# Kernel optimization log

Measured on AMD Instinct MI355X. Metric: run time of the kernel, lower is better.

The kernel has to match this reference:

```python
import jax, jax.numpy as jnp
import numpy as np

EPS = 1e-6
NUM_HEADS = 8
HEAD_DIM = 64


def _elu_plus_one(x):
    # ELU(x) + 1 : positive feature map used for linear attention
    return jax.nn.elu(x) + 1.0


def setup_inputs() -> dict:
    key = jax.random.key(0)
    ks = jax.random.split(key, 10)
    B, S, D = 1, 4096, 512  # batch, seq_len, hidden_size
    P = NUM_HEADS * HEAD_DIM  # proj_dim == hidden_size here
    scale = 0.05  # keep projections numerically tame
    return {
        "hidden_states": jax.random.normal(ks[0], (B, S, D), jnp.float32),
        "Wq": jax.random.normal(ks[1], (D, P), jnp.float32) * scale,
        "bq": jnp.zeros((P,), jnp.float32),
        "Wk": jax.random.normal(ks[2], (D, P), jnp.float32) * scale,
        "bk": jnp.zeros((P,), jnp.float32),
        "Wv": jax.random.normal(ks[3], (D, P), jnp.float32) * scale,
        "bv": jnp.zeros((P,), jnp.float32),
        "Wo": jax.random.normal(ks[4], (P, D), jnp.float32) * scale,
        # persistent per-head tensor-product memory: M [H, Dh, Dh], z [H, Dh]
        "M_mem": jax.random.uniform(ks[5], (NUM_HEADS, HEAD_DIM, HEAD_DIM), jnp.float32),
        "z_mem": jax.random.uniform(ks[6], (NUM_HEADS, HEAD_DIM), jnp.float32),
    }


def reference(hidden_states, Wq, bq, Wk, bk, Wv, bv, Wo, M_mem, z_mem):
    B, S, D = hidden_states.shape
    H, Dh = NUM_HEADS, HEAD_DIM

    def split_heads(t):
        # [B, S, H*Dh] -> [B, H, S, Dh]
        return t.reshape(B, S, H, Dh).transpose(0, 2, 1, 3)

    q = split_heads(hidden_states @ Wq + bq)
    k = split_heads(hidden_states @ Wk + bk)
    v = split_heads(hidden_states @ Wv + bv)

    sq = _elu_plus_one(q)  # sigma(Q)  [B,H,S,Dh]
    sk = _elu_plus_one(k)  # sigma(K)  [B,H,S,Dh]

    # kv[t] = sigma(k_t) (x) v_t ; causal prefix sums, seeded by persistent memory
    kv = sk[..., :, None] * v[..., None, :]            # [B,H,S,Dh,Dh]
    cumsum_kv = jnp.cumsum(kv, axis=2) + M_mem[None, :, None]  # + M per head
    cumsum_k = jnp.cumsum(sk, axis=2) + z_mem[None, :, None]   # + z per head

    numerator = jnp.einsum('bhsd,bhsde->bhse', sq, cumsum_kv)  # [B,H,S,Dh]
    denominator = jnp.einsum('bhsd,bhsd->bhs', sq, cumsum_k)   # [B,H,S]
    out = numerator / (denominator[..., None] + EPS)

    out = out.transpose(0, 2, 1, 3).reshape(B, S, H * Dh)  # merge heads
    return out @ Wo
```

## Files before the change

kernel.cpp:

```cpp
#include <hip/hip_runtime.h>
#include <hip/hip_bf16.h>
#include <math.h>

#define S_LEN 4096
#define D_HID 512
#define P_DIM 512
#define H_NUM 8
#define DH 64
#define NC 64
#define EPS 1e-6f

typedef __attribute__((ext_vector_type(8))) short short8;
typedef __attribute__((ext_vector_type(4))) float f32x4;
typedef __attribute__((ext_vector_type(4))) unsigned short ushort4v;

static __device__ __forceinline__ float b2f(unsigned short u) {
  return __builtin_bit_cast(float, ((unsigned int)u) << 16);
}
static __device__ __forceinline__ unsigned short f2b(float f) {
  unsigned int u = __builtin_bit_cast(unsigned int, f);
  u = (u + 0x7fff + ((u >> 16) & 1)) >> 16;
  return (unsigned short)u;
}
static __device__ __forceinline__ int swz(int row, int d) {
  return d ^ ((row & 7) << 3);
}

#define GLOAD_LDS16(g, l)                                              \
  __builtin_amdgcn_global_load_lds(                                    \
      (const __attribute__((address_space(1))) unsigned int*)(g),      \
      (__attribute__((address_space(3))) unsigned int*)(l), 16, 0, 0)

#define MFMA16(a, b, c) __builtin_amdgcn_mfma_f32_16x16x32_bf16(a, b, c, 0, 0, 0)

#define VMCNT0 asm volatile("s_waitcnt vmcnt(0)" ::: "memory")

__global__ __launch_bounds__(256) void prep_kernel(
    const float* __restrict__ hs, const float* __restrict__ Wq,
    const float* __restrict__ Wk, const float* __restrict__ Wv,
    const float* __restrict__ Wo, unsigned short* __restrict__ hs_bf,
    unsigned short* __restrict__ WT) {
  __shared__ float t[32][33];
  int bid = blockIdx.x, tid = threadIdx.x;
  if (bid < 2048) {
    int idx = bid * 256 + tid;
    float4 v = ((const float4*)hs)[idx];
    ushort4v o = {f2b(v.x), f2b(v.y), f2b(v.z), f2b(v.w)};
    *(ushort4v*)(hs_bf + (size_t)idx * 4) = o;
  } else {
    int b2 = bid - 2048;
    int z = b2 >> 8, r = b2 & 255;
    const float* src = (z == 0) ? Wq : (z == 1) ? Wk : (z == 2) ? Wv : Wo;
    int bx = (r & 15) * 32;
    int by = (r >> 4) * 32;
    int lx = tid & 31, ly = tid >> 5;
#pragma unroll
    for (int i = 0; i < 4; i++)
      t[ly + i * 8][lx] = src[(size_t)(by + ly + i * 8) * 512 + bx + lx];
    __syncthreads();
#pragma unroll
    for (int i = 0; i < 4; i++) {
      int n = bx + ly + i * 8;
      WT[((size_t)z * 512 + n) * 512 + by + lx] = f2b(t[lx][ly + i * 8]);
    }
  }
}

__global__ __launch_bounds__(256) void proj_kernel(
    const unsigned short* __restrict__ hs_bf,
    const unsigned short* __restrict__ WT, const float* __restrict__ bq,
    const float* __restrict__ bk, const float* __restrict__ bv,
    unsigned short* __restrict__ sqz, unsigned short* __restrict__ skz,
    unsigned short* __restrict__ vTz, float* __restrict__ KVt,
    float* __restrict__ ksum) {
  union U {
    struct {
      unsigned short As[2][64 * 32];
      unsigned short Bs[2][192 * 32];
    } st;
    struct {
      unsigned short skT[64 * 64];
      unsigned short vT[64 * 64];
    } cs;
  };
  __shared__ U u;
  int tid = threadIdx.x, w = tid >> 6, lane = tid & 63;
  int c = blockIdx.x, h = blockIdx.y;
  int fr = lane & 15, kg8 = (lane >> 4) * 8, q4 = (lane >> 4) * 4;
  int ldrow = lane >> 2, ldk = (lane & 3) * 8;

  const unsigned short* Ag =
      hs_bf + (size_t)(c * 64 + w * 16 + ldrow) * 512 + ldk;
  const unsigned short* Bg =
      WT + (size_t)(h * 64 + w * 16 + ldrow) * 512 + ldk;

#define PSTAGE(buf, k0)                                              \
  do {                                                               \
    GLOAD_LDS16(Ag + (k0), u.st.As[buf] + w * 512);                  \
    GLOAD_LDS16(Bg + (k0), u.st.Bs[buf] + w * 512);                  \
    GLOAD_LDS16(Bg + 262144 + (k0), u.st.Bs[buf] + 2048 + w * 512);  \
    GLOAD_LDS16(Bg + 524288 + (k0), u.st.Bs[buf] + 4096 + w * 512);  \
  } while (0)

  f32x4 acc[12] = {};
  PSTAGE(0, 0);
  VMCNT0;
  __builtin_amdgcn_s_barrier();
  int cur = 0;
  for (int it = 0; it < 16; it++) {
    if (it < 15) PSTAGE(cur ^ 1, (it + 1) * 32);
    short8 a = *(const short8*)(u.st.As[cur] + (w * 16 + fr) * 32 + kg8);
#pragma unroll
    for (int nt = 0; nt < 12; nt++) {
      short8 b = *(const short8*)(u.st.Bs[cur] + (nt * 16 + fr) * 32 + kg8);
      acc[nt] = MFMA16(a, b, acc[nt]);
    }
    VMCNT0;
    __builtin_amdgcn_s_barrier();
    cur ^= 1;
  }

#pragma unroll
  for (int nt = 0; nt < 12; nt++) {
    int z = nt >> 2, d = (nt & 3) * 16 + fr;
    float bias = (z == 0) ? bq[h * 64 + d]
                          : (z == 1) ? bk[h * 64 + d] : bv[h * 64 + d];
#pragma unroll
    for (int j = 0; j < 4; j++) {
      int t = w * 16 + q4 + j;
      int s = c * 64 + t;
      float val = acc[nt][j] + bias;
      if (z < 2) val = (val > 0.f) ? (val + 1.f) : __expf(val);
      unsigned short bb = f2b(val);
      if (z == 0) {
        sqz[((size_t)h * S_LEN + s) * 64 + swz(s, d)] = bb;
      } else if (z == 1) {
        skz[((size_t)h * S_LEN + s) * 64 + swz(s, d)] = bb;
        u.cs.skT[d * 64 + swz(d, t)] = bb;
      } else {
        u.cs.vT[d * 64 + swz(d, t)] = bb;
      }
    }
  }
  __syncthreads();

#pragma unroll
  for (int i = 0; i < 2; i++) {
    int G = tid + 256 * i;
    int e = G >> 3, gq = G & 7;
    *(short8*)(vTz + ((size_t)(h * 64 + e)) * S_LEN + c * 64 + gq * 8) =
        *(const short8*)(u.cs.vT + e * 64 + gq * 8);
  }

  {
    short8 onesA = {};
    if (fr == 0) {
#pragma unroll
      for (int j = 0; j < 8; j++) onesA[j] = (short)0x3F80;
    }
    f32x4 accC[4] = {}, accKk[4] = {};
#pragma unroll
    for (int k0 = 0; k0 < 64; k0 += 32) {
      int e = w * 16 + fr;
      short8 a2 =
          *(const short8*)(u.cs.vT + e * 64 + ((k0 + kg8) ^ ((e & 7) << 3)));
#pragma unroll
      for (int nt = 0; nt < 4; nt++) {
        int d = nt * 16 + fr;
        short8 b2 = *(const short8*)(u.cs.skT + d * 64 +
                                     ((k0 + kg8) ^ ((d & 7) << 3)));
        accC[nt] = MFMA16(a2, b2, accC[nt]);
        if (w == 0) accKk[nt] = MFMA16(onesA, b2, accKk[nt]);
      }
    }
    size_t base = (size_t)(h * NC + c) * 4096;
    int e0 = w * 16 + q4;
#pragma unroll
    for (int nt = 0; nt < 4; nt++)
#pragma unroll
      for (int j = 0; j < 4; j++)
        KVt[base + (size_t)(e0 + j) * 64 + nt * 16 + fr] = accC[nt][j];
    if (w == 0 && lane < 16) {
#pragma unroll
      for (int nt = 0; nt < 4; nt++)
        ksum[(size_t)(h * NC + c) * 64 + nt * 16 + lane] = accKk[nt][0];
    }
  }
#undef PSTAGE
}

__global__ __launch_bounds__(256) void prefix2_kernel(
    const float* __restrict__ KVt, const float* __restrict__ ksum,
    const float* __restrict__ M_mem, const float* __restrict__ z_mem,
    unsigned short* __restrict__ KVpz, unsigned short* __restrict__ zp_bf) {
  __shared__ float p[64 * 4];
  __shared__ float zz[64 * 4];
  int h = blockIdx.x >> 6, seg = blockIdx.x & 63;
  int tid = threadIdx.x;
  int d = tid & 63, q = tid >> 6;
  size_t ebase = (size_t)h * NC * 4096 + (size_t)seg * 64 + d;
  float part = 0.f;
#pragma unroll 4
  for (int i = 0; i < 16; i++)
    part += KVt[ebase + (size_t)(q * 16 + i) * 4096];
  p[d * 4 + q] = part;
  if (seg == 0) {
    size_t zb = (size_t)h * NC * 64 + d;
    float pz = 0.f;
#pragma unroll 4
    for (int i = 0; i < 16; i++) pz += ksum[zb + (size_t)(q * 16 + i) * 64];
    zz[d * 4 + q] = pz;
  }
  __syncthreads();
  float pref = M_mem[h * 4096 + d * 64 + seg];
  for (int q2 = 0; q2 < q; q2++) pref += p[d * 4 + q2];
  int sw = swz(seg, d);
#pragma unroll 4
  for (int i = 0; i < 16; i++) {
    int cc = q * 16 + i;
    KVpz[(size_t)(h * NC + cc) * 4096 + seg * 64 + sw] = f2b(pref);
    pref += KVt[ebase + (size_t)cc * 4096];
  }
  if (seg == 0) {
    float bz = z_mem[h * 64 + d];
    for (int q2 = 0; q2 < q; q2++) bz += zz[d * 4 + q2];
    size_t zb = (size_t)h * NC * 64 + d;
#pragma unroll 4
    for (int i = 0; i < 16; i++) {
      int cc = q * 16 + i;
      zp_bf[zb + (size_t)cc * 64] = f2b(bz);
      bz += ksum[zb + (size_t)cc * 64];
    }
  }
}

__global__ __launch_bounds__(256) void attn_mfma(
    const unsigned short* __restrict__ sqz, const unsigned short* __restrict__ skz,
    const unsigned short* __restrict__ vTz, const unsigned short* __restrict__ KVpz,
    const unsigned short* __restrict__ zp_bf, unsigned short* __restrict__ attnb) {
  __shared__ unsigned short sq_lds[4096], sk_lds[4096];
  __shared__ unsigned short btv_lds[80 * 64], btm_lds[80 * 64];
  __shared__ unsigned short shi_lds[4096], slo_lds[4096];
  int h = blockIdx.x / NC, c = blockIdx.x % NC;
  int tid = threadIdx.x, w = tid >> 6, lane = tid & 63;

  {
    const unsigned short* sq_g = sqz + ((size_t)h * S_LEN + c * 64) * 64;
    const unsigned short* sk_g = skz + ((size_t)h * S_LEN + c * 64) * 64;
    const unsigned short* km_g = KVpz + (size_t)(h * NC + c) * 4096;
    int lr = lane >> 3, lc = (lane & 7) * 8;
#pragma unroll
    for (int i = 0; i < 2; i++) {
      int seg = w * 2 + i;
      GLOAD_LDS16(sq_g + seg * 512 + lane * 8, sq_lds + seg * 512);
      GLOAD_LDS16(sk_g + seg * 512 + lane * 8, sk_lds + seg * 512);
      GLOAD_LDS16(km_g + seg * 512 + lane * 8, btm_lds + seg * 512);
      GLOAD_LDS16(vTz + ((size_t)h * 64 + seg * 8 + lr) * S_LEN + c * 64 + lc,
                  btv_lds + seg * 512);
    }
  }
  if (tid < 8) {
    short8 one;
#pragma unroll
    for (int j = 0; j < 8; j++) one[j] = (short)0x3F80;
    *(short8*)(btv_lds + 64 * 64 + tid * 8) = one;
    *(short8*)(btm_lds + 64 * 64 + tid * 8) =
        *(const short8*)(zp_bf + (size_t)(h * NC + c) * 64 + tid * 8);
  }
  __syncthreads();

  int fr = lane & 15, kg8 = (lane >> 4) * 8;
  int ta = w * 16 + fr;
  int sw_a = (ta & 7) << 3;

  f32x4 accS[4] = {};
#pragma unroll
  for (int k0 = 0; k0 < 64; k0 += 32) {
    short8 a = *(const short8*)(sq_lds + ta * 64 + ((k0 + kg8) ^ sw_a));
#pragma unroll
    for (int nt = 0; nt < 4; nt++) {
      int tp = nt * 16 + fr;
      short8 b =
          *(const short8*)(sk_lds + tp * 64 + ((k0 + kg8) ^ ((tp & 7) << 3)));
      accS[nt] = MFMA16(a, b, accS[nt]);
    }
  }
  int r0 = (lane >> 4) * 4;
#pragma unroll
  for (int nt = 0; nt < 4; nt++) {
    int tp = nt * 16 + fr;
#pragma unroll
    for (int j = 0; j < 4; j++) {
      int t = w * 16 + r0 + j;
      float s = (tp <= t) ? accS[nt][j] : 0.f;
      unsigned short hi = f2b(s);
      unsigned short lo = f2b(s - b2f(hi));
      shi_lds[t * 64 + swz(t, tp)] = hi;
      slo_lds[t * 64 + swz(t, tp)] = lo;
    }
  }
  f32x4 acc2[5] = {};
#pragma unroll
  for (int ks = 0; ks < 6; ks++) {
    const unsigned short* asrc = (ks < 2) ? shi_lds : (ks < 4) ? slo_lds : sq_lds;
    const unsigned short* bsrc = (ks < 4) ? btv_lds : btm_lds;
    int ak = (ks & 1) * 32 + kg8;
    short8 a = *(const short8*)(asrc + ta * 64 + (ak ^ sw_a));
#pragma unroll
    for (int nt = 0; nt < 5; nt++) {
      int n = nt * 16 + fr;
      short8 b = *(const short8*)(bsrc + n * 64 + (ak ^ ((n & 7) << 3)));
      acc2[nt] = MFMA16(a, b, acc2[nt]);
    }
  }
  float inv[4];
#pragma unroll
  for (int j = 0; j < 4; j++) {
    float dj = __shfl(acc2[4][j], (lane & 48), 64);
    inv[j] = 1.f / (dj + EPS);
  }
  int srow = c * 64 + w * 16 + r0;
#pragma unroll
  for (int nt = 0; nt < 4; nt++) {
    int col = h * 64 + nt * 16 + fr;
#pragma unroll
    for (int j = 0; j < 4; j++)
      attnb[(size_t)(srow + j) * 512 + col] = f2b(acc2[nt][j] * inv[j]);
  }
}

__global__ __launch_bounds__(256) void gemm_out(
    const unsigned short* __restrict__ A, const unsigned short* __restrict__ BT,
    float* __restrict__ outf) {
  __shared__ unsigned short As[2][64 * 32];
  __shared__ unsigned short Bs[2][128 * 32];
  int tid = threadIdx.x, w = tid >> 6, lane = tid & 63;
  int bm = blockIdx.x * 64, bn = blockIdx.y * 128;
  f32x4 acc[2][4] = {};
  int ldrow = lane >> 2, ldk = (lane & 3) * 8;
  int wr = w >> 1, wc = w & 1;
  int fr = lane & 15, kg8 = (lane >> 4) * 8, q4 = (lane >> 4) * 4;
  const unsigned short* Ag = A + (size_t)(bm + w * 16 + ldrow) * 512 + ldk;
  const unsigned short* Bg0 = BT + (size_t)(bn + w * 16 + ldrow) * 512 + ldk;
  const unsigned short* Bg1 =
      BT + (size_t)(bn + (w + 4) * 16 + ldrow) * 512 + ldk;

#define OSTAGE(buf, k0)                              \
  do {                                               \
    GLOAD_LDS16(Ag + (k0), As[buf] + w * 512);       \
    GLOAD_LDS16(Bg0 + (k0), Bs[buf] + w * 512);      \
    GLOAD_LDS16(Bg1 + (k0), Bs[buf] + (w + 4) * 512); \
  } while (0)

  OSTAGE(0, 0);
  VMCNT0;
  __builtin_amdgcn_s_barrier();
  int cur = 0;
  for (int it = 0; it < 16; it++) {
    if (it < 15) OSTAGE(cur ^ 1, (it + 1) * 32);
    short8 a[2], b[4];
#pragma unroll
    for (int m = 0; m < 2; m++)
      a[m] = *(const short8*)(As[cur] + (wr * 32 + m * 16 + fr) * 32 + kg8);
#pragma unroll
    for (int n = 0; n < 4; n++)
      b[n] = *(const short8*)(Bs[cur] + (wc * 64 + n * 16 + fr) * 32 + kg8);
#pragma unroll
    for (int m = 0; m < 2; m++)
#pragma unroll
      for (int n = 0; n < 4; n++) acc[m][n] = MFMA16(a[m], b[n], acc[m][n]);
    VMCNT0;
    __builtin_amdgcn_s_barrier();
    cur ^= 1;
  }
#pragma unroll
  for (int m = 0; m < 2; m++) {
    int sl0 = wr * 32 + m * 16 + q4;
#pragma unroll
    for (int n = 0; n < 4; n++) {
      int col = bn + wc * 64 + n * 16 + fr;
#pragma unroll
      for (int j = 0; j < 4; j++)
        outf[(size_t)(bm + sl0 + j) * 512 + col] = acc[m][n][j];
    }
  }
#undef OSTAGE
}

extern "C" void kernel_launch(void* const* d_in, const int* in_sizes, int n_in,
                              void* d_out, int out_size, void* d_ws,
                              size_t ws_size, hipStream_t stream) {
  const float* hs = (const float*)d_in[0];
  const float* Wq = (const float*)d_in[1];
  const float* bq = (const float*)d_in[2];
  const float* Wk = (const float*)d_in[3];
  const float* bk = (const float*)d_in[4];
  const float* Wv = (const float*)d_in[5];
  const float* bv = (const float*)d_in[6];
  const float* Wo = (const float*)d_in[7];
  const float* M_mem = (const float*)d_in[8];
  const float* z_mem = (const float*)d_in[9];
  float* out = (float*)d_out;

  unsigned short* hs_bf = (unsigned short*)d_ws;
  unsigned short* WT = hs_bf + (size_t)S_LEN * D_HID;
  unsigned short* sqz = WT + (size_t)4 * 512 * 512;
  unsigned short* skz = sqz + (size_t)H_NUM * S_LEN * DH;
  unsigned short* vTz = skz + (size_t)H_NUM * S_LEN * DH;
  unsigned short* attnb = vTz + (size_t)H_NUM * S_LEN * DH;
  unsigned short* KVpz = attnb + (size_t)S_LEN * P_DIM;
  unsigned short* zp_bf = KVpz + (size_t)H_NUM * NC * DH * DH;
  float* KVt = (float*)(zp_bf + (size_t)H_NUM * NC * DH);
  float* ksum = KVt + (size_t)H_NUM * NC * DH * DH;

  prep_kernel<<<3072, 256, 0, stream>>>(hs, Wq, Wk, Wv, Wo, hs_bf, WT);

  proj_kernel<<<dim3(NC, H_NUM), 256, 0, stream>>>(hs_bf, WT, bq, bk, bv, sqz,
                                                   skz, vTz, KVt, ksum);

  prefix2_kernel<<<512, 256, 0, stream>>>(KVt, ksum, M_mem, z_mem, KVpz, zp_bf);

  attn_mfma<<<512, 256, 0, stream>>>(sqz, skz, vTz, KVpz, zp_bf, attnb);

  gemm_out<<<dim3(S_LEN / 64, 512 / 128), 256, 0, stream>>>(
      attnb, WT + (size_t)3 * 512 * 512, out);
}
```

Measured before the change: 121.1 us.

## Fuse projection, prefix, attention and output GEMM into one persistent kernel

Merges the projection, chunk prefix-sum, intra-chunk attention and output GEMM kernels into one 512-block kernel separated by software grid barriers built on atomics. sq/sk/vT tiles stay in LDS between the projection and attention phases, so their global round-trip is removed, and three kernel launch gaps go away. The projection tile is re-split across warps as 2x6 MFMA tiles and the output GEMM uses 64x64 tiles. The grid barrier assumes all 512 blocks are co-resident, which risks deadlock if occupancy does not allow it. The barriers also serialise phases with spin-waiting.

```diff
diff --git a/kernel.cpp b/kernel.cpp
--- a/kernel.cpp
+++ b/kernel.cpp
@@ -9,6 +9,7 @@
 #define DH 64
 #define NC 64
 #define EPS 1e-6f
+#define NBLK 512
 
 typedef __attribute__((ext_vector_type(8))) short short8;
 typedef __attribute__((ext_vector_type(4))) float f32x4;
@@ -35,13 +36,33 @@
 
 #define VMCNT0 asm volatile("s_waitcnt vmcnt(0)" ::: "memory")
 
+static __device__ __forceinline__ void grid_bar(unsigned* sync, int k) {
+  __syncthreads();
+  if (threadIdx.x == 0) {
+    __threadfence();
+    unsigned prev = __hip_atomic_fetch_add(sync + k, 1u, __ATOMIC_ACQ_REL,
+                                           __HIP_MEMORY_SCOPE_AGENT);
+    if (prev == (unsigned)(NBLK - 1)) {
+      __hip_atomic_store(sync + 4 + k, 1u, __ATOMIC_RELEASE,
+                         __HIP_MEMORY_SCOPE_AGENT);
+    } else {
+      while (__hip_atomic_load(sync + 4 + k, __ATOMIC_ACQUIRE,
+                               __HIP_MEMORY_SCOPE_AGENT) == 0u) {
+        __builtin_amdgcn_s_sleep(2);
+      }
+    }
+  }
+  __syncthreads();
+}
+
 __global__ __launch_bounds__(256) void prep_kernel(
     const float* __restrict__ hs, const float* __restrict__ Wq,
     const float* __restrict__ Wk, const float* __restrict__ Wv,
     const float* __restrict__ Wo, unsigned short* __restrict__ hs_bf,
-    unsigned short* __restrict__ WT) {
+    unsigned short* __restrict__ WT, unsigned* __restrict__ sync) {
   __shared__ float t[32][33];
   int bid = blockIdx.x, tid = threadIdx.x;
+  if (bid == 0 && tid < 8) sync[tid] = 0u;
   if (bid < 2048) {
     int idx = bid * 256 + tid;
     float4 v = ((const float4*)hs)[idx];
@@ -66,93 +87,104 @@
   }
 }
 
-__global__ __launch_bounds__(256) void proj_kernel(
+__global__ __launch_bounds__(256) void fused_kernel(
     const unsigned short* __restrict__ hs_bf,
     const unsigned short* __restrict__ WT, const float* __restrict__ bq,
     const float* __restrict__ bk, const float* __restrict__ bv,
-    unsigned short* __restrict__ sqz, unsigned short* __restrict__ skz,
-    unsigned short* __restrict__ vTz, float* __restrict__ KVt,
-    float* __restrict__ ksum) {
-  union U {
-    struct {
-      unsigned short As[2][64 * 32];
-      unsigned short Bs[2][192 * 32];
-    } st;
-    struct {
-      unsigned short skT[64 * 64];
-      unsigned short vT[64 * 64];
-    } cs;
-  };
-  __shared__ U u;
-  int tid = threadIdx.x, w = tid >> 6, lane = tid & 63;
-  int c = blockIdx.x, h = blockIdx.y;
+    const float* __restrict__ M_mem, const float* __restrict__ z_mem,
+    float* __restrict__ KVt, float* __restrict__ ksum,
+    unsigned short* __restrict__ KVpz, unsigned short* __restrict__ zp_bf,
+    unsigned short* __restrict__ attnb, float* __restrict__ outf,
+    unsigned* __restrict__ sync) {
+  __shared__ unsigned short sqL[64 * 64];
+  __shared__ unsigned short skL[64 * 64];
+  __shared__ unsigned short vTL[80 * 64];
+  __shared__ unsigned short uraw[16384];
+
+  int bid = blockIdx.x, tid = threadIdx.x;
+  int w = tid >> 6, lane = tid & 63;
+  int h = bid & 7, c = bid >> 3;
   int fr = lane & 15, kg8 = (lane >> 4) * 8, q4 = (lane >> 4) * 4;
   int ldrow = lane >> 2, ldk = (lane & 3) * 8;
-
-  const unsigned short* Ag =
-      hs_bf + (size_t)(c * 64 + w * 16 + ldrow) * 512 + ldk;
-  const unsigned short* Bg =
-      WT + (size_t)(h * 64 + w * 16 + ldrow) * 512 + ldk;
-
-#define PSTAGE(buf, k0)                                              \
-  do {                                                               \
-    GLOAD_LDS16(Ag + (k0), u.st.As[buf] + w * 512);                  \
-    GLOAD_LDS16(Bg + (k0), u.st.Bs[buf] + w * 512);                  \
-    GLOAD_LDS16(Bg + 262144 + (k0), u.st.Bs[buf] + 2048 + w * 512);  \
-    GLOAD_LDS16(Bg + 524288 + (k0), u.st.Bs[buf] + 4096 + w * 512);  \
+  int wr = w >> 1, wc = w & 1;
+
+  {
+    const unsigned short* Ag =
+        hs_bf + (size_t)(c * 64 + w * 16 + ldrow) * 512 + ldk;
+    const unsigned short* Bg =
+        WT + (size_t)(h * 64 + w * 16 + ldrow) * 512 + ldk;
+#define PSTAGE(buf, k0)                                                   \
+  do {                                                                    \
+    GLOAD_LDS16(Ag + (k0), uraw + (buf)*2048 + w * 512);                  \
+    GLOAD_LDS16(Bg + (k0), uraw + 4096 + (buf)*6144 + w * 512);           \
+    GLOAD_LDS16(Bg + 262144 + (k0), uraw + 4096 + (buf)*6144 + 2048 + w * 512); \
+    GLOAD_LDS16(Bg + 524288 + (k0), uraw + 4096 + (buf)*6144 + 4096 + w * 512); \
   } while (0)
 
-  f32x4 acc[12] = {};
-  PSTAGE(0, 0);
-  VMCNT0;
-  __builtin_amdgcn_s_barrier();
-  int cur = 0;
-  for (int it = 0; it < 16; it++) {
-    if (it < 15) PSTAGE(cur ^ 1, (it + 1) * 32);
-    short8 a = *(const short8*)(u.st.As[cur] + (w * 16 + fr) * 32 + kg8);
-#pragma unroll
-    for (int nt = 0; nt < 12; nt++) {
-      short8 b = *(const short8*)(u.st.Bs[cur] + (nt * 16 + fr) * 32 + kg8);
-      acc[nt] = MFMA16(a, b, acc[nt]);
-    }
+    f32x4 acc[2][6] = {};
+    PSTAGE(0, 0);
     VMCNT0;
     __builtin_amdgcn_s_barrier();
-    cur ^= 1;
-  }
-
-#pragma unroll
-  for (int nt = 0; nt < 12; nt++) {
-    int z = nt >> 2, d = (nt & 3) * 16 + fr;
-    float bias = (z == 0) ? bq[h * 64 + d]
-                          : (z == 1) ? bk[h * 64 + d] : bv[h * 64 + d];
-#pragma unroll
-    for (int j = 0; j < 4; j++) {
-      int t = w * 16 + q4 + j;
-      int s = c * 64 + t;
-      float val = acc[nt][j] + bias;
-      if (z < 2) val = (val > 0.f) ? (val + 1.f) : __expf(val);
-      unsigned short bb = f2b(val);
-      if (z == 0) {
-        sqz[((size_t)h * S_LEN + s) * 64 + swz(s, d)] = bb;
-      } else if (z == 1) {
-        skz[((size_t)h * S_LEN + s) * 64 + swz(s, d)] = bb;
-        u.cs.skT[d * 64 + swz(d, t)] = bb;
-      } else {
-        u.cs.vT[d * 64 + swz(d, t)] = bb;
-      }
-    }
-  }
-  __syncthreads();
-
-#pragma unroll
-  for (int i = 0; i < 2; i++) {
-    int G = tid + 256 * i;
-    int e = G >> 3, gq = G & 7;
-    *(short8*)(vTz + ((size_t)(h * 64 + e)) * S_LEN + c * 64 + gq * 8) =
-        *(const short8*)(u.cs.vT + e * 64 + gq * 8);
-  }
-
-  {
+    int cur = 0;
+    for (int it = 0; it < 16; it++) {
+      if (it < 15) PSTAGE(cur ^ 1, (it + 1) * 32);
+      short8 a[2], b[6];
+#pragma unroll
+      for (int m = 0; m < 2; m++)
+        a[m] = *(const short8*)(uraw + cur * 2048 +
+                                (wr * 32 + m * 16 + fr) * 32 + kg8);
+#pragma unroll
+      for (int n = 0; n < 6; n++)
+        b[n] = *(const short8*)(uraw + 4096 + cur * 6144 +
+                                (wc * 96 + n * 16 + fr) * 32 + kg8);
+#pragma unroll
+      for (int m = 0; m < 2; m++)
+#pragma unroll
+        for (int n = 0; n < 6; n++) acc[m][n] = MFMA16(a[m], b[n], acc[m][n]);
+      VMCNT0;
+      __builtin_amdgcn_s_barrier();
+      cur ^= 1;
+    }
+#undef PSTAGE
+
+    unsigned short* skT = uraw;
+#pragma unroll
+    for (int n = 0; n < 6; n++) {
+      int cl = wc * 96 + n * 16 + fr;
+      int z = cl >> 6, d = cl & 63;
+      float bias = (z == 0) ? bq[h * 64 + d]
+                            : (z == 1) ? bk[h * 64 + d] : bv[h * 64 + d];
+#pragma unroll
+      for (int m = 0; m < 2; m++) {
+#pragma unroll
+        for (int j = 0; j < 4; j++) {
+          int t = wr * 32 + m * 16 + q4 + j;
+          float val = acc[m][n][j] + bias;
+          if (z < 2) val = (val > 0.f) ? (val + 1.f) : __expf(val);
+          unsigned short bb = f2b(val);
+          if (z == 0) {
+            sqL[t * 64 + swz(t, d)] = bb;
+          } else if (z == 1) {
+            skL[t * 64 + swz(t, d)] = bb;
+            skT[d * 64 + swz(d, t)] = bb;
+          } else {
+            vTL[d * 64 + swz(d, t)] = bb;
+          }
+        }
+      }
+    }
+    if (tid < 8) {
+      short8 one;
+#pragma unroll
+      for (int j = 0; j < 8; j++) one[j] = (short)0x3F80;
+      *(short8*)(vTL + 64 * 64 + tid * 8) = one;
+    }
+    if (tid < 120) {
+      short8 zz = {};
+      *(short8*)(vTL + 65 * 64 + tid * 8) = zz;
+    }
+    __syncthreads();
+
     short8 onesA = {};
     if (fr == 0) {
 #pragma unroll
@@ -163,12 +195,12 @@
     for (int k0 = 0; k0 < 64; k0 += 32) {
       int e = w * 16 + fr;
       short8 a2 =
-          *(const short8*)(u.cs.vT + e * 64 + ((k0 + kg8) ^ ((e & 7) << 3)));
+          *(const short8*)(vTL + e * 64 + ((k0 + kg8) ^ ((e & 7) << 3)));
 #pragma unroll
       for (int nt = 0; nt < 4; nt++) {
         int d = nt * 16 + fr;
-        short8 b2 = *(const short8*)(u.cs.skT + d * 64 +
-                                     ((k0 + kg8) ^ ((d & 7) << 3)));
+        short8 b2 =
+            *(const short8*)(skT + d * 64 + ((k0 + kg8) ^ ((d & 7) << 3)));
         accC[nt] = MFMA16(a2, b2, accC[nt]);
         if (w == 0) accKk[nt] = MFMA16(onesA, b2, accKk[nt]);
       }
@@ -186,205 +218,175 @@
         ksum[(size_t)(h * NC + c) * 64 + nt * 16 + lane] = accKk[nt][0];
     }
   }
-#undef PSTAGE
-}
-
-__global__ __launch_bounds__(256) void prefix2_kernel(
-    const float* __restrict__ KVt, const float* __restrict__ ksum,
-    const float* __restrict__ M_mem, const float* __restrict__ z_mem,
-    unsigned short* __restrict__ KVpz, unsigned short* __restrict__ zp_bf) {
-  __shared__ float p[64 * 4];
-  __shared__ float zz[64 * 4];
-  int h = blockIdx.x >> 6, seg = blockIdx.x & 63;
-  int tid = threadIdx.x;
-  int d = tid & 63, q = tid >> 6;
-  size_t ebase = (size_t)h * NC * 4096 + (size_t)seg * 64 + d;
-  float part = 0.f;
+
+  grid_bar(sync, 0);
+
+  {
+    float* p = (float*)uraw;
+    float* zz = p + 256;
+    int h2 = bid >> 6, seg = bid & 63;
+    int d = tid & 63, q = tid >> 6;
+    size_t ebase = (size_t)h2 * NC * 4096 + (size_t)seg * 64 + d;
+    float part = 0.f;
 #pragma unroll 4
-  for (int i = 0; i < 16; i++)
-    part += KVt[ebase + (size_t)(q * 16 + i) * 4096];
-  p[d * 4 + q] = part;
-  if (seg == 0) {
-    size_t zb = (size_t)h * NC * 64 + d;
-    float pz = 0.f;
+    for (int i = 0; i < 16; i++)
+      part += KVt[ebase + (size_t)(q * 16 + i) * 4096];
+    p[d * 4 + q] = part;
+    if (seg == 0) {
+      size_t zb = (size_t)h2 * NC * 64 + d;
+      float pz = 0.f;
 #pragma unroll 4
-    for (int i = 0; i < 16; i++) pz += ksum[zb + (size_t)(q * 16 + i) * 64];
-    zz[d * 4 + q] = pz;
-  }
-  __syncthreads();
-  float pref = M_mem[h * 4096 + d * 64 + seg];
-  for (int q2 = 0; q2 < q; q2++) pref += p[d * 4 + q2];
-  int sw = swz(seg, d);
-#pragma unroll 4
-  for (int i = 0; i < 16; i++) {
-    int cc = q * 16 + i;
-    KVpz[(size_t)(h * NC + cc) * 4096 + seg * 64 + sw] = f2b(pref);
-    pref += KVt[ebase + (size_t)cc * 4096];
-  }
-  if (seg == 0) {
-    float bz = z_mem[h * 64 + d];
-    for (int q2 = 0; q2 < q; q2++) bz += zz[d * 4 + q2];
-    size_t zb = (size_t)h * NC * 64 + d;
+      for (int i = 0; i < 16; i++) pz += ksum[zb + (size_t)(q * 16 + i) * 64];
+      zz[d * 4 + q] = pz;
+    }
+    __syncthreads();
+    float pref = M_mem[h2 * 4096 + d * 64 + seg];
+    for (int q2 = 0; q2 < q; q2++) pref += p[d * 4 + q2];
+    int sw = swz(seg, d);
 #pragma unroll 4
     for (int i = 0; i < 16; i++) {
       int cc = q * 16 + i;
-      zp_bf[zb + (size_t)cc * 64] = f2b(bz);
-      bz += ksum[zb + (size_t)cc * 64];
-    }
-  }
-}
-
-__global__ __launch_bounds__(256) void attn_mfma(
-    const unsigned short* __restrict__ sqz, const unsigned short* __restrict__ skz,
-    const unsigned short* __restrict__ vTz, const unsigned short* __restrict__ KVpz,
-    const unsigned short* __restrict__ zp_bf, unsigned short* __restrict__ attnb) {
-  __shared__ unsigned short sq_lds[4096], sk_lds[4096];
-  __shared__ unsigned short btv_lds[80 * 64], btm_lds[80 * 64];
-  __shared__ unsigned short shi_lds[4096], slo_lds[4096];
-  int h = blockIdx.x / NC, c = blockIdx.x % NC;
-  int tid = threadIdx.x, w = tid >> 6, lane = tid & 63;
+      KVpz[(size_t)(h2 * NC + cc) * 4096 + seg * 64 + sw] = f2b(pref);
+      pref += KVt[ebase + (size_t)cc * 4096];
+    }
+    if (seg == 0) {
+      float bz = z_mem[h2 * 64 + d];
+      for (int q2 = 0; q2 < q; q2++) bz += zz[d * 4 + q2];
+      size_t zb = (size_t)h2 * NC * 64 + d;
+#pragma unroll 4
+      for (int i = 0; i < 16; i++) {
+        int cc = q * 16 + i;
+        zp_bf[zb + (size_t)cc * 64] = f2b(bz);
+        bz += ksum[zb + (size_t)cc * 64];
+      }
+    }
+  }
+
+  grid_bar(sync, 1);
 
   {
-    const unsigned short* sq_g = sqz + ((size_t)h * S_LEN + c * 64) * 64;
-    const unsigned short* sk_g = skz + ((size_t)h * S_LEN + c * 64) * 64;
+    unsigned short* btm = uraw;
+    unsigned short* shi = uraw + 5120;
+    unsigned short* slo = uraw + 9216;
     const unsigned short* km_g = KVpz + (size_t)(h * NC + c) * 4096;
-    int lr = lane >> 3, lc = (lane & 7) * 8;
 #pragma unroll
     for (int i = 0; i < 2; i++) {
-      int seg = w * 2 + i;
-      GLOAD_LDS16(sq_g + seg * 512 + lane * 8, sq_lds + seg * 512);
-      GLOAD_LDS16(sk_g + seg * 512 + lane * 8, sk_lds + seg * 512);
-      GLOAD_LDS16(km_g + seg * 512 + lane * 8, btm_lds + seg * 512);
-      GLOAD_LDS16(vTz + ((size_t)h * 64 + seg * 8 + lr) * S_LEN + c * 64 + lc,
-                  btv_lds + seg * 512);
-    }
-  }
-  if (tid < 8) {
-    short8 one;
-#pragma unroll
-    for (int j = 0; j < 8; j++) one[j] = (short)0x3F80;
-    *(short8*)(btv_lds + 64 * 64 + tid * 8) = one;
-    *(short8*)(btm_lds + 64 * 64 + tid * 8) =
-        *(const short8*)(zp_bf + (size_t)(h * NC + c) * 64 + tid * 8);
-  }
-  __syncthreads();
-
-  int fr = lane & 15, kg8 = (lane >> 4) * 8;
-  int ta = w * 16 + fr;
-  int sw_a = (ta & 7) << 3;
-
-  f32x4 accS[4] = {};
-#pragma unroll
-  for (int k0 = 0; k0 < 64; k0 += 32) {
-    short8 a = *(const short8*)(sq_lds + ta * 64 + ((k0 + kg8) ^ sw_a));
+      int seg2 = w * 2 + i;
+      GLOAD_LDS16(km_g + seg2 * 512 + lane * 8, btm + seg2 * 512);
+    }
+    if (tid < 8)
+      *(short8*)(btm + 64 * 64 + tid * 8) =
+          *(const short8*)(zp_bf + (size_t)(h * NC + c) * 64 + tid * 8);
+
+    int ta = w * 16 + fr, sw_a = (ta & 7) << 3;
+    f32x4 accS[4] = {};
+#pragma unroll
+    for (int k0 = 0; k0 < 64; k0 += 32) {
+      short8 a = *(const short8*)(sqL + ta * 64 + ((k0 + kg8) ^ sw_a));
+#pragma unroll
+      for (int nt = 0; nt < 4; nt++) {
+        int tp = nt * 16 + fr;
+        short8 b =
+            *(const short8*)(skL + tp * 64 + ((k0 + kg8) ^ ((tp & 7) << 3)));
+        accS[nt] = MFMA16(a, b, accS[nt]);
+      }
+    }
 #pragma unroll
     for (int nt = 0; nt < 4; nt++) {
       int tp = nt * 16 + fr;
-      short8 b =
-          *(const short8*)(sk_lds + tp * 64 + ((k0 + kg8) ^ ((tp & 7) << 3)));
-      accS[nt] = MFMA16(a, b, accS[nt]);
-    }
-  }
-  int r0 = (lane >> 4) * 4;
-#pragma unroll
-  for (int nt = 0; nt < 4; nt++) {
-    int tp = nt * 16 + fr;
+#pragma unroll
+      for (int j = 0; j < 4; j++) {
+        int t = w * 16 + q4 + j;
+        float s = (tp <= t) ? accS[nt][j] : 0.f;
+        unsigned short hi = f2b(s);
+        unsigned short lo = f2b(s - b2f(hi));
+        shi[t * 64 + swz(t, tp)] = hi;
+        slo[t * 64 + swz(t, tp)] = lo;
+      }
+    }
+    __syncthreads();
+    f32x4 acc2[5] = {};
+#pragma unroll
+    for (int ks = 0; ks < 6; ks++) {
+      const unsigned short* asrc = (ks < 2) ? shi : (ks < 4) ? slo : sqL;
+      const unsigned short* bsrc = (ks < 4) ? vTL : btm;
+      int ak = (ks & 1) * 32 + kg8;
+      short8 a = *(const short8*)(asrc + ta * 64 + (ak ^ sw_a));
+#pragma unroll
+      for (int nt = 0; nt < 5; nt++) {
+        int n = nt * 16 + fr;
+        short8 b = *(const short8*)(bsrc + n * 64 + (ak ^ ((n & 7) << 3)));
+        acc2[nt] = MFMA16(a, b, acc2[nt]);
+      }
+    }
+    float inv[4];
 #pragma unroll
     for (int j = 0; j < 4; j++) {
-      int t = w * 16 + r0 + j;
-      float s = (tp <= t) ? accS[nt][j] : 0.f;
-      unsigned short hi = f2b(s);
-      unsigned short lo = f2b(s - b2f(hi));
-      shi_lds[t * 64 + swz(t, tp)] = hi;
-      slo_lds[t * 64 + swz(t, tp)] = lo;
-    }
-  }
-  f32x4 acc2[5] = {};
-#pragma unroll
-  for (int ks = 0; ks < 6; ks++) {
-    const unsigned short* asrc = (ks < 2) ? shi_lds : (ks < 4) ? slo_lds : sq_lds;
-    const unsigned short* bsrc = (ks < 4) ? btv_lds : btm_lds;
-    int ak = (ks & 1) * 32 + kg8;
-    short8 a = *(const short8*)(asrc + ta * 64 + (ak ^ sw_a));
-#pragma unroll
-    for (int nt = 0; nt < 5; nt++) {
-      int n = nt * 16 + fr;
-      short8 b = *(const short8*)(bsrc + n * 64 + (ak ^ ((n & 7) << 3)));
-      acc2[nt] = MFMA16(a, b, acc2[nt]);
-    }
-  }
-  float inv[4];
-#pragma unroll
-  for (int j = 0; j < 4; j++) {
-    float dj = __shfl(acc2[4][j], (lane & 48), 64);
-    inv[j] = 1.f / (dj + EPS);
-  }
-  int srow = c * 64 + w * 16 + r0;
-#pragma unroll
-  for (int nt = 0; nt < 4; nt++) {
-    int col = h * 64 + nt * 16 + fr;
-#pragma unroll
-    for (int j = 0; j < 4; j++)
-      attnb[(size_t)(srow + j) * 512 + col] = f2b(acc2[nt][j] * inv[j]);
-  }
-}
-
-__global__ __launch_bounds__(256) void gemm_out(
-    const unsigned short* __restrict__ A, const unsigned short* __restrict__ BT,
-    float* __restrict__ outf) {
-  __shared__ unsigned short As[2][64 * 32];
-  __shared__ unsigned short Bs[2][128 * 32];
-  int tid = threadIdx.x, w = tid >> 6, lane = tid & 63;
-  int bm = blockIdx.x * 64, bn = blockIdx.y * 128;
-  f32x4 acc[2][4] = {};
-  int ldrow = lane >> 2, ldk = (lane & 3) * 8;
-  int wr = w >> 1, wc = w & 1;
-  int fr = lane & 15, kg8 = (lane >> 4) * 8, q4 = (lane >> 4) * 4;
-  const unsigned short* Ag = A + (size_t)(bm + w * 16 + ldrow) * 512 + ldk;
-  const unsigned short* Bg0 = BT + (size_t)(bn + w * 16 + ldrow) * 512 + ldk;
-  const unsigned short* Bg1 =
-      BT + (size_t)(bn + (w + 4) * 16 + ldrow) * 512 + ldk;
-
-#define OSTAGE(buf, k0)                              \
-  do {                                               \
-    GLOAD_LDS16(Ag + (k0), As[buf] + w * 512);       \
-    GLOAD_LDS16(Bg0 + (k0), Bs[buf] + w * 512);      \
-    GLOAD_LDS16(Bg1 + (k0), Bs[buf] + (w + 4) * 512); \
+      float dj = __shfl(acc2[4][j], (lane & 48), 64);
+      inv[j] = 1.f / (dj + EPS);
+    }
+    int srow = c * 64 + w * 16 + q4;
+#pragma unroll
+    for (int nt = 0; nt < 4; nt++) {
+      int col = h * 64 + nt * 16 + fr;
+#pragma unroll
+      for (int j = 0; j < 4; j++)
+        attnb[(size_t)(srow + j) * 512 + col] = f2b(acc2[nt][j] * inv[j]);
+    }
+  }
+
+  grid_bar(sync, 2);
+
+  {
+    int bm = (bid >> 3) * 64, bn = (bid & 7) * 64;
+    const unsigned short* WoT = WT + (size_t)3 * 512 * 512;
+    const unsigned short* Ag =
+        attnb + (size_t)(bm + w * 16 + ldrow) * 512 + ldk;
+    const unsigned short* Bg =
+        WoT + (size_t)(bn + w * 16 + ldrow) * 512 + ldk;
+#define OSTAGE(buf, k0)                                          \
+  do {                                                           \
+    GLOAD_LDS16(Ag + (k0), uraw + (buf)*2048 + w * 512);         \
+    GLOAD_LDS16(Bg + (k0), uraw + 4096 + (buf)*2048 + w * 512);  \
   } while (0)
 
-  OSTAGE(0, 0);
-  VMCNT0;
-  __builtin_amdgcn_s_barrier();
-  int cur = 0;
-  for (int it = 0; it < 16; it++) {
-    if (it < 15) OSTAGE(cur ^ 1, (it + 1) * 32);
-    short8 a[2], b[4];
-#pragma unroll
-    for (int m = 0; m < 2; m++)
-      a[m] = *(const short8*)(As[cur] + (wr * 32 + m * 16 + fr) * 32 + kg8);
-#pragma unroll
-    for (int n = 0; n < 4; n++)
-      b[n] = *(const short8*)(Bs[cur] + (wc * 64 + n * 16 + fr) * 32 + kg8);
-#pragma unroll
-    for (int m = 0; m < 2; m++)
-#pragma unroll
-      for (int n = 0; n < 4; n++) acc[m][n] = MFMA16(a[m], b[n], acc[m][n]);
+    f32x4 acc4[2][2] = {};
+    OSTAGE(0, 0);
     VMCNT0;
     __builtin_amdgcn_s_barrier();
-    cur ^= 1;
-  }
-#pragma unroll
-  for (int m = 0; m < 2; m++) {
-    int sl0 = wr * 32 + m * 16 + q4;
-#pragma unroll
-    for (int n = 0; n < 4; n++) {
-      int col = bn + wc * 64 + n * 16 + fr;
-#pragma unroll
-      for (int j = 0; j < 4; j++)
-        outf[(size_t)(bm + sl0 + j) * 512 + col] = acc[m][n][j];
-    }
-  }
+    int cur = 0;
+    for (int it = 0; it < 16; it++) {
+      if (it < 15) OSTAGE(cur ^ 1, (it + 1) * 32);
+      short8 a[2], b[2];
+#pragma unroll
+      for (int m = 0; m < 2; m++)
+        a[m] = *(const short8*)(uraw + cur * 2048 +
+                                (wr * 32 + m * 16 + fr) * 32 + kg8);
+#pragma unroll
+      for (int n = 0; n < 2; n++)
+        b[n] = *(const short8*)(uraw + 4096 + cur * 2048 +
+                                (wc * 32 + n * 16 + fr) * 32 + kg8);
+#pragma unroll
+      for (int m = 0; m < 2; m++)
+#pragma unroll
+        for (int n = 0; n < 2; n++) acc4[m][n] = MFMA16(a[m], b[n], acc4[m][n]);
+      VMCNT0;
+      __builtin_amdgcn_s_barrier();
+      cur ^= 1;
+    }
 #undef OSTAGE
+#pragma unroll
+    for (int m = 0; m < 2; m++) {
+      int row0 = bm + wr * 32 + m * 16 + q4;
+#pragma unroll
+      for (int n = 0; n < 2; n++) {
+        int col = bn + wc * 32 + n * 16 + fr;
+#pragma unroll
+        for (int j = 0; j < 4; j++)
+          outf[(size_t)(row0 + j) * 512 + col] = acc4[m][n][j];
+      }
+    }
+  }
 }
 
 extern "C" void kernel_launch(void* const* d_in, const int* in_sizes, int n_in,
@@ -404,24 +406,16 @@
 
   unsigned short* hs_bf = (unsigned short*)d_ws;
   unsigned short* WT = hs_bf + (size_t)S_LEN * D_HID;
-  unsigned short* sqz = WT + (size_t)4 * 512 * 512;
-  unsigned short* skz = sqz + (size_t)H_NUM * S_LEN * DH;
-  unsigned short* vTz = skz + (size_t)H_NUM * S_LEN * DH;
-  unsigned short* attnb = vTz + (size_t)H_NUM * S_LEN * DH;
+  unsigned short* attnb = WT + (size_t)4 * 512 * 512;
   unsigned short* KVpz = attnb + (size_t)S_LEN * P_DIM;
   unsigned short* zp_bf = KVpz + (size_t)H_NUM * NC * DH * DH;
   float* KVt = (float*)(zp_bf + (size_t)H_NUM * NC * DH);
   float* ksum = KVt + (size_t)H_NUM * NC * DH * DH;
-
-  prep_kernel<<<3072, 256, 0, stream>>>(hs, Wq, Wk, Wv, Wo, hs_bf, WT);
-
-  proj_kernel<<<dim3(NC, H_NUM), 256, 0, stream>>>(hs_bf, WT, bq, bk, bv, sqz,
-                                                   skz, vTz, KVt, ksum);
-
-  prefix2_kernel<<<512, 256, 0, stream>>>(KVt, ksum, M_mem, z_mem, KVpz, zp_bf);
-
-  attn_mfma<<<512, 256, 0, stream>>>(sqz, skz, vTz, KVpz, zp_bf, attnb);
-
-  gemm_out<<<dim3(S_LEN / 64, 512 / 128), 256, 0, stream>>>(
-      attnb, WT + (size_t)3 * 512 * 512, out);
-}
+  unsigned* sync = (unsigned*)(ksum + (size_t)H_NUM * NC * DH);
+
+  prep_kernel<<<3072, 256, 0, stream>>>(hs, Wq, Wk, Wv, Wo, hs_bf, WT, sync);
+
+  fused_kernel<<<NBLK, 256, 0, stream>>>(hs_bf, WT, bq, bk, bv, M_mem, z_mem,
+                                         KVt, ksum, KVpz, zp_bf, attnb, out,
+                                         sync);
+}
```

Measured after the change: 284.3 us. 135% more time.
